# Kernel tuning notes

Hardware: AMD Instinct MI355X
Metric: run time of the kernel (lower is better)

Reference implementation:

```python
import jax, jax.numpy as jnp
import numpy as np
from jax import lax
from jax.scipy.special import logsumexp

LOG2PI = 1.8378770664093453

def _gauss_lp(x, mean, logvar):
    return -0.5 * ((x - mean) ** 2 * jnp.exp(-logvar) + logvar + LOG2PI)

def setup_inputs() -> dict:
    key = jax.random.key(0)
    ks = jax.random.split(key, 12)
    B, T, D, H, X, K, U = 32, 1024, 512, 512, 32, 8, 2
    s = 0.05
    return {
        'ys': jax.random.normal(ks[0], (B, T, D), jnp.float32),
        'us': jax.random.normal(ks[1], (B, T, U), jnp.float32),
        'eps': jax.random.normal(ks[2], (B, T, X), jnp.float32),
        'W1': jax.random.normal(ks[3], (D, H), jnp.float32) * s,
        'b1': jnp.zeros((H,), jnp.float32),
        'Wmu': jax.random.normal(ks[4], (H, X), jnp.float32) * s,
        'bmu': jnp.zeros((X,), jnp.float32),
        'Wlv': jax.random.normal(ks[5], (H, X), jnp.float32) * s,
        'blv': jnp.zeros((X,), jnp.float32),
        'Wz': jax.random.normal(ks[6], (X, K * K), jnp.float32) * s,
        'bz': jnp.zeros((K * K,), jnp.float32),
        'A': jax.random.normal(ks[7], (K, X, X), jnp.float32) * s,
        'Bu': jax.random.normal(ks[8], (K, U, X), jnp.float32) * s,
        'bx': jnp.zeros((K, X), jnp.float32),
        'x_logvar': jnp.zeros((K, X), jnp.float32),
        'x0_mean': jax.random.normal(ks[9], (K, X), jnp.float32) * s,
        'x0_logvar': jnp.zeros((K, X), jnp.float32),
        'C': jax.random.normal(ks[10], (X, D), jnp.float32) * s,
        'd': jnp.zeros((D,), jnp.float32),
        'y_logvar': jnp.zeros((D,), jnp.float32),
        'log_init_z': jnp.zeros((K,), jnp.float32),
    }

def _forward_backward(log_a, log_b, log_init):
    # log_a: [B,T,K,K] with log_a[:,t,j,k] = log p(z_t=j | z_{t-1}=k); log_b: [B,T,K]
    B, T, K = log_b.shape
    la = jnp.moveaxis(log_a[:, 1:], 1, 0)  # [T-1,B,K,K]
    lb = jnp.moveaxis(log_b[:, 1:], 1, 0)  # [T-1,B,K]
    a0 = log_init[None, :] + log_b[:, 0]
    c0 = logsumexp(a0, axis=-1)
    a0 = a0 - c0[:, None]
    def fstep(alpha, ab):
        la_t, lb_t = ab
        a = lb_t + logsumexp(la_t + alpha[:, None, :], axis=-1)
        c = logsumexp(a, axis=-1)
        an = a - c[:, None]
        return an, (an, c)
    _, (alphas, cs) = lax.scan(fstep, a0, (la, lb))
    log_px = c0 + jnp.sum(cs, axis=0)  # [B] log marginal likelihood
    fwd = jnp.concatenate([a0[None], alphas], axis=0)  # [T,B,K]
    betaT = jnp.zeros((B, K), log_b.dtype)
    def bstep(beta, ab):
        la_t, lb_t = ab
        b = logsumexp(la_t + (lb_t + beta)[:, :, None], axis=1)  # sum over next-state j
        b = b - logsumexp(b, axis=-1, keepdims=True)
        return b, b
    _, betas = lax.scan(bstep, betaT, (la, lb), reverse=True)
    bwd = jnp.concatenate([betas, betaT[None]], axis=0)  # [T,B,K]
    lg = fwd + bwd
    log_gamma1 = lg - logsumexp(lg, axis=-1, keepdims=True)
    return jnp.moveaxis(log_gamma1, 0, 1), log_px

def reference(ys, us, eps, W1, b1, Wmu, bmu, Wlv, blv, Wz, bz, A, Bu, bx,
              x_logvar, x0_mean, x0_logvar, C, d, y_logvar, log_init_z):
    B, T, D = ys.shape
    K, X = x0_mean.shape
    # inference net q(x|y): per-step MLP producing Gaussian, reparameterized sample
    h = jnp.tanh(ys @ W1 + b1)
    mu = h @ Wmu + bmu
    lv = h @ Wlv + blv
    x = mu + jnp.exp(0.5 * lv) * eps                        # [B,T,X]
    x_entropy = 0.5 * jnp.sum(eps ** 2 + lv + LOG2PI, -1)   # -log q(x^), [B,T]
    # discrete transition log p(z_t | z_{t-1}, x_{t-1}) with log(eye) prepended at t=0
    logits = (x[:, :-1] @ Wz + bz).reshape(B, T - 1, K, K)
    log_a_t = jax.nn.log_softmax(logits, axis=-2)           # normalize_logprob axis=-2
    log_eye = jnp.log(jnp.eye(K, dtype=ys.dtype) + 1e-10)[None, None]
    log_a = jnp.concatenate([jnp.broadcast_to(log_eye, (B, 1, K, K)), log_a_t], axis=1)
    # continuous likelihood log p(x_t | x_{t-1}, u_t, z_t=k) -> [B,T,K]
    log_b0 = jnp.sum(_gauss_lp(x[:, 0, None, :], x0_mean, x0_logvar), -1)  # [B,K]
    means = (jnp.einsum('btd,kde->btke', x[:, :-1], A)
             + jnp.einsum('btu,kue->btke', us[:, 1:], Bu) + bx)            # [B,T-1,K,X]
    log_bt = jnp.sum(_gauss_lp(x[:, 1:, None, :], means, x_logvar), -1)
    log_b = jnp.concatenate([log_b0[:, None], log_bt], axis=1)
    log_init = jax.nn.log_softmax(log_init_z)
    log_gamma1, log_px = _forward_backward(log_a, log_b, log_init)
    # posterior-weighted generated mean mixed over states, then emission
    xt1_gen = jnp.sum(means * jnp.exp(log_gamma1[:, 1:, :, None]), axis=-2)
    x_gen1 = jnp.concatenate([x[:, :1], xt1_gen], axis=1)
    y_mean = x_gen1 @ C + d
    log_py = jnp.sum(_gauss_lp(ys, y_mean, y_logvar), -1)   # [B,T]
    log_p_xy = log_px + jnp.sum(log_py, -1)                 # [B]
    log_qx = jnp.mean(jnp.sum(x_entropy, 1))
    elbo = jnp.mean(log_p_xy) + log_qx
    return elbo
```

## Files before the change

kernel.cpp:

```cpp
#include <hip/hip_runtime.h>
#include <math.h>

#define LOG2PI 1.8378770664093453f

#define NB 32
#define NT 1024
#define ND 512
#define NH 512
#define NX 32
#define NK 8
#define NU 2

#define NCH 93
#define CHL 11

typedef __attribute__((ext_vector_type(8))) short bf16x8;
typedef __attribute__((ext_vector_type(4))) float f32x4;

__device__ __forceinline__ unsigned short f2bf(float f) {
    unsigned u = __float_as_uint(f);
    unsigned r = (u + 0x7FFF + ((u >> 16) & 1)) >> 16;
    return (unsigned short)r;
}

__device__ __forceinline__ unsigned pack_bf2(float a, float b) {
    unsigned ua = __float_as_uint(a) + 0x8000u;
    unsigned ub = __float_as_uint(b) + 0x8000u;
    return __builtin_amdgcn_perm(ub, ua, 0x07060302);
}

__device__ __forceinline__ float tanh_fast(float v) {
    float t = __expf(2.0f * v);
    return 1.0f - 2.0f * __builtin_amdgcn_rcpf(t + 1.0f);
}

#define DPP_X1 0xB1
#define DPP_X2 0x4E
#define DPP_X3 0x1B
#define DPP_X7 0x141

template <int CTRL>
__device__ __forceinline__ float dppx(float v) {
    return __int_as_float(__builtin_amdgcn_update_dpp(
        0, __float_as_int(v), CTRL, 0xF, 0xF, true));
}

__device__ __forceinline__ float fb_matvec(float4 a0, float4 a1, float v) {
    float p1 = dppx<DPP_X1>(v);
    float p2 = dppx<DPP_X2>(v);
    float p3 = dppx<DPP_X3>(v);
    float p7 = dppx<DPP_X7>(v);
    float p4 = dppx<DPP_X7>(p3);
    float p5 = dppx<DPP_X7>(p2);
    float p6 = dppx<DPP_X7>(p1);
    float c0 = fmaf(a0.y, p1, a0.x * v);
    float c1 = fmaf(a0.w, p3, a0.z * p2);
    float c2 = fmaf(a1.y, p5, a1.x * p4);
    float c3 = fmaf(a1.w, p7, a1.z * p6);
    return (c0 + c1) + (c2 + c3);
}

__device__ __forceinline__ float fb_matvecT(float4 a0, float4 a1, float w) {
    float q0 = a0.x * w;
    float t1 = dppx<DPP_X1>(a0.y * w);
    float t2 = dppx<DPP_X2>(a0.z * w);
    float t3 = dppx<DPP_X3>(a0.w * w);
    float t7 = dppx<DPP_X7>(a1.w * w);
    float t4 = dppx<DPP_X7>(dppx<DPP_X3>(a1.x * w));
    float t5 = dppx<DPP_X7>(dppx<DPP_X2>(a1.y * w));
    float t6 = dppx<DPP_X7>(dppx<DPP_X1>(a1.z * w));
    return ((q0 + t1) + (t2 + t3)) + ((t4 + t5) + (t6 + t7));
}

__device__ __forceinline__ float gsum8(float v) {
    float s = v + dppx<DPP_X1>(v);
    s = s + dppx<DPP_X2>(s);
    s = s + dppx<DPP_X7>(dppx<DPP_X3>(s));
    return s;
}

__device__ __forceinline__ float max8(float4 l0, float4 l1) {
    return fmaxf(fmaxf(fmaxf(l0.x, l0.y), fmaxf(l0.z, l0.w)),
                 fmaxf(fmaxf(l1.x, l1.y), fmaxf(l1.z, l1.w)));
}

__device__ __forceinline__ float lse8_high(float v) {
    float m = v;
    m = fmaxf(m, __shfl_xor(m, 8, 64));
    m = fmaxf(m, __shfl_xor(m, 16, 64));
    m = fmaxf(m, __shfl_xor(m, 32, 64));
    float s = __expf(v - m);
    s += __shfl_xor(s, 8, 64);
    s += __shfl_xor(s, 16, 64);
    s += __shfl_xor(s, 32, 64);
    return m + __logf(s);
}

__global__ __launch_bounds__(256) void k_prep_w(
    const float* __restrict__ W1, const float* __restrict__ Wmu,
    const float* __restrict__ Wlv, const float* __restrict__ C,
    const float* __restrict__ dvec, const float* __restrict__ ylv,
    unsigned short* __restrict__ WT, unsigned short* __restrict__ wmlv,
    unsigned short* __restrict__ W2bf, float* __restrict__ G,
    float* __restrict__ c2x, float* __restrict__ ivbuf)
{
    __shared__ float tile[32][33];
    const int bid = blockIdx.x;
    const int tid = threadIdx.x;
    if (bid < 256) {
        const int bx = (bid & 15) * 32;
        const int by = (bid >> 4) * 32;
        const int tx = tid & 31, ty = tid >> 5;
        for (int i = ty; i < 32; i += 8)
            tile[i][tx] = W1[(size_t)(bx + i) * 512 + by + tx];
        __syncthreads();
        for (int i = ty; i < 32; i += 8)
            WT[(size_t)(by + i) * 512 + bx + tx] = f2bf(tile[tx][i]);
        return;
    }
    if (bid < 288) {
        const int t = bid - 256;
        const float* W = (t >> 4) ? Wlv : Wmu;
        const int base = (t >> 4) * 32;
        const int g = t & 15;
        const int tx = tid & 31, ty = tid >> 5;
        for (int i = ty; i < 32; i += 8)
            tile[i][tx] = W[(size_t)(g * 32 + i) * 32 + tx];
        __syncthreads();
        for (int i = ty; i < 32; i += 8)
            wmlv[(size_t)(base + i) * 512 + g * 32 + tx] = f2bf(tile[tx][i]);
        return;
    }
    if (bid == 320) {
        for (int i = tid; i < 32 * 512; i += 256)
            W2bf[i] = f2bf(C[i] * __expf(-ylv[i & 511]));
        ivbuf[tid] = __expf(-ylv[tid]);
        ivbuf[tid + 256] = __expf(-ylv[tid + 256]);
        return;
    }
    const int x = bid - 288;
    const int y = tid >> 3, seg = tid & 7;
    const float* Cx = &C[(size_t)x * 512];
    const float* Cy = &C[(size_t)y * 512];
    float p = 0.f;
    for (int j = 0; j < 64; ++j) {
        int dcol = seg * 64 + j;
        p = fmaf(Cx[dcol] * __expf(-ylv[dcol]), Cy[dcol], p);
    }
    p = gsum8(p);
    if (seg == 0) G[x * 33 + y] = p;
    if (tid < 8) {
        float q = 0.f;
        for (int j = 0; j < 64; ++j) {
            int dcol = tid * 64 + j;
            q = fmaf(Cx[dcol] * __expf(-ylv[dcol]), dvec[dcol], q);
        }
        q = gsum8(q);
        if (tid == 0) c2x[x] = q;
    }
}

__global__ __launch_bounds__(256) void k_gemm_h_mfma(
    const float* __restrict__ ys,
    const unsigned short* __restrict__ Bbf,
    const float* __restrict__ b1, unsigned short* __restrict__ hb)
{
    __shared__ unsigned short As[128 * 64];
    __shared__ unsigned short Bs[128 * 64];
    const int tid = threadIdx.x;
    const int bm = blockIdx.x * 128;
    const int bn = blockIdx.y * 128;
    const int wid = tid >> 6, lane = tid & 63;
    const int wm = wid >> 1, wn = wid & 1;

    f32x4 acc[4][4];
#pragma unroll
    for (int m = 0; m < 4; ++m)
#pragma unroll
        for (int n = 0; n < 4; ++n)
            acc[m][n] = (f32x4){0.f, 0.f, 0.f, 0.f};

    for (int k0 = 0; k0 < 512; k0 += 64) {
#pragma unroll
        for (int r = 0; r < 4; ++r) {
            int l = tid + r * 256;
            int row = l >> 3, c8 = l & 7;
            int sidx = row * 8 + (c8 ^ (row & 7));
            const float4 f0 = *reinterpret_cast<const float4*>(
                &ys[(size_t)(bm + row) * 512 + k0 + c8 * 8]);
            const float4 f1 = *reinterpret_cast<const float4*>(
                &ys[(size_t)(bm + row) * 512 + k0 + c8 * 8 + 4]);
            uint4 ua;
            ua.x = pack_bf2(f0.x, f0.y);
            ua.y = pack_bf2(f0.z, f0.w);
            ua.z = pack_bf2(f1.x, f1.y);
            ua.w = pack_bf2(f1.z, f1.w);
            *reinterpret_cast<uint4*>(&As[sidx * 8]) = ua;
            uint4 vb = *reinterpret_cast<const uint4*>(
                &Bbf[(size_t)(bn + row) * 512 + k0 + c8 * 8]);
            *reinterpret_cast<uint4*>(&Bs[sidx * 8]) = vb;
        }
        __syncthreads();
#pragma unroll
        for (int kh = 0; kh < 2; ++kh) {
            bf16x8 af[4], bfr[4];
            const int c8r = kh * 4 + (lane >> 4);
#pragma unroll
            for (int m = 0; m < 4; ++m) {
                int rA = wm * 64 + m * 16 + (lane & 15);
                af[m] = *reinterpret_cast<bf16x8*>(
                    &As[rA * 64 + (c8r ^ (rA & 7)) * 8]);
            }
#pragma unroll
            for (int n = 0; n < 4; ++n) {
                int rB = wn * 64 + n * 16 + (lane & 15);
                bfr[n] = *reinterpret_cast<bf16x8*>(
                    &Bs[rB * 64 + (c8r ^ (rB & 7)) * 8]);
            }
#pragma unroll
            for (int m = 0; m < 4; ++m)
#pragma unroll
                for (int n = 0; n < 4; ++n)
                    acc[m][n] = __builtin_amdgcn_mfma_f32_16x16x32_bf16(
                        af[m], bfr[n], acc[m][n], 0, 0, 0);
        }
        __syncthreads();
    }
    float b1v[4];
#pragma unroll
    for (int n = 0; n < 4; ++n)
        b1v[n] = b1[bn + wn * 64 + n * 16 + (lane & 15)];
#pragma unroll
    for (int m = 0; m < 4; ++m) {
#pragma unroll
        for (int q = 0; q < 4; ++q) {
            int row = bm + wm * 64 + m * 16 + (lane >> 4) * 4 + q;
#pragma unroll
            for (int n = 0; n < 4; ++n) {
                int col = bn + wn * 64 + n * 16 + (lane & 15);
                hb[(size_t)row * 512 + col] =
                    f2bf(tanh_fast(acc[m][n][q] + b1v[n]));
            }
        }
    }
}

__global__ __launch_bounds__(256) void k_proj(
    const float* __restrict__ ys, const unsigned short* __restrict__ W2bf,
    const float* __restrict__ dvec, const float* __restrict__ ivbuf,
    float* __restrict__ proj, float* __restrict__ term1)
{
    __shared__ unsigned short As[128 * 64];
    __shared__ unsigned short Bs[32 * 64];
    const int tid = threadIdx.x;
    const int bm = blockIdx.x * 128;
    const int wid = tid >> 6, lane = tid & 63;
    const int c8 = tid & 7;
    f32x4 acc[2][2];
#pragma unroll
    for (int m = 0; m < 2; ++m)
#pragma unroll
        for (int n = 0; n < 2; ++n)
            acc[m][n] = (f32x4){0.f, 0.f, 0.f, 0.f};
    float t1p[4] = {0.f, 0.f, 0.f, 0.f};

    for (int k0 = 0; k0 < 512; k0 += 64) {
        const float4 dv0 = *reinterpret_cast<const float4*>(&dvec[k0 + c8 * 8]);
        const float4 dv1 = *reinterpret_cast<const float4*>(&dvec[k0 + c8 * 8 + 4]);
        const float4 iv0 = *reinterpret_cast<const float4*>(&ivbuf[k0 + c8 * 8]);
        const float4 iv1 = *reinterpret_cast<const float4*>(&ivbuf[k0 + c8 * 8 + 4]);
#pragma unroll
        for (int r = 0; r < 4; ++r) {
            int l = tid + r * 256;
            int row = l >> 3;
            int sidx = row * 8 + (c8 ^ (row & 7));
            const float4 f0 = *reinterpret_cast<const float4*>(
                &ys[(size_t)(bm + row) * 512 + k0 + c8 * 8]);
            const float4 f1 = *reinterpret_cast<const float4*>(
                &ys[(size_t)(bm + row) * 512 + k0 + c8 * 8 + 4]);
            float g0 = f0.x - dv0.x, g1 = f0.y - dv0.y;
            float g2 = f0.z - dv0.z, g3 = f0.w - dv0.w;
            float g4 = f1.x - dv1.x, g5 = f1.y - dv1.y;
            float g6 = f1.z - dv1.z, g7 = f1.w - dv1.w;
            t1p[r] += (g0 * g0 * iv0.x + g1 * g1 * iv0.y)
                    + (g2 * g2 * iv0.z + g3 * g3 * iv0.w)
                    + (g4 * g4 * iv1.x + g5 * g5 * iv1.y)
                    + (g6 * g6 * iv1.z + g7 * g7 * iv1.w);
            uint4 ua;
            ua.x = pack_bf2(f0.x, f0.y);
            ua.y = pack_bf2(f0.z, f0.w);
            ua.z = pack_bf2(f1.x, f1.y);
            ua.w = pack_bf2(f1.z, f1.w);
            *reinterpret_cast<uint4*>(&As[sidx * 8]) = ua;
        }
        {
            int row = tid >> 3;
            int sidx = row * 8 + (c8 ^ (row & 7));
            uint4 v = *reinterpret_cast<const uint4*>(
                &W2bf[(size_t)row * 512 + k0 + c8 * 8]);
            *reinterpret_cast<uint4*>(&Bs[sidx * 8]) = v;
        }
        __syncthreads();
#pragma unroll
        for (int kh = 0; kh < 2; ++kh) {
            const int c8r = kh * 4 + (lane >> 4);
            bf16x8 af[2], bfr[2];
#pragma unroll
            for (int m = 0; m < 2; ++m) {
                int rA = wid * 32 + m * 16 + (lane & 15);
                af[m] = *reinterpret_cast<bf16x8*>(
                    &As[rA * 64 + (c8r ^ (rA & 7)) * 8]);
            }
#pragma unroll
            for (int n = 0; n < 2; ++n) {
                int rB = n * 16 + (lane & 15);
                bfr[n] = *reinterpret_cast<bf16x8*>(
                    &Bs[rB * 64 + (c8r ^ (rB & 7)) * 8]);
            }
#pragma unroll
            for (int m = 0; m < 2; ++m)
#pragma unroll
                for (int n = 0; n < 2; ++n)
                    acc[m][n] = __builtin_amdgcn_mfma_f32_16x16x32_bf16(
                        af[m], bfr[n], acc[m][n], 0, 0, 0);
        }
        __syncthreads();
    }
#pragma unroll
    for (int m = 0; m < 2; ++m)
#pragma unroll
        for (int q = 0; q < 4; ++q) {
            int row = bm + wid * 32 + m * 16 + (lane >> 4) * 4 + q;
#pragma unroll
            for (int n = 0; n < 2; ++n) {
                int col = n * 16 + (lane & 15);
                proj[(size_t)row * 32 + col] = acc[m][n][q];
            }
        }
#pragma unroll
    for (int r = 0; r < 4; ++r) {
        float s = gsum8(t1p[r]);
        if ((tid & 7) == 0) term1[bm + (tid >> 3) + r * 32] = s;
    }
}

__global__ __launch_bounds__(256) void k_mulv_mfma(
    const unsigned short* __restrict__ hbf,
    const unsigned short* __restrict__ Wt,
    const float* __restrict__ bmu, const float* __restrict__ blv,
    const float* __restrict__ eps,
    float* __restrict__ x, float* __restrict__ xent)
{
    __shared__ unsigned short As[128 * 64];
    __shared__ unsigned short Bs[64 * 64];
    const int tid = threadIdx.x;
    const int bm = blockIdx.x * 128;
    const int wid = tid >> 6, lane = tid & 63;
    f32x4 acc[2][4];
#pragma unroll
    for (int m = 0; m < 2; ++m)
#pragma unroll
        for (int n = 0; n < 4; ++n)
            acc[m][n] = (f32x4){0.f, 0.f, 0.f, 0.f};

    for (int k0 = 0; k0 < 512; k0 += 64) {
#pragma unroll
        for (int r = 0; r < 4; ++r) {
            int l = tid + r * 256, row = l >> 3, c8 = l & 7;
            int sidx = row * 8 + (c8 ^ (row & 7));
            uint4 v = *reinterpret_cast<const uint4*>(
                &hbf[(size_t)(bm + row) * 512 + k0 + c8 * 8]);
            *reinterpret_cast<uint4*>(&As[sidx * 8]) = v;
        }
#pragma unroll
        for (int r = 0; r < 2; ++r) {
            int l = tid + r * 256, row = l >> 3, c8 = l & 7;
            int sidx = row * 8 + (c8 ^ (row & 7));
            uint4 v = *reinterpret_cast<const uint4*>(
                &Wt[(size_t)row * 512 + k0 + c8 * 8]);
            *reinterpret_cast<uint4*>(&Bs[sidx * 8]) = v;
        }
        __syncthreads();
#pragma unroll
        for (int kh = 0; kh < 2; ++kh) {
            const int c8r = kh * 4 + (lane >> 4);
            bf16x8 af[2], bfr[4];
#pragma unroll
            for (int m = 0; m < 2; ++m) {
                int rA = wid * 32 + m * 16 + (lane & 15);
                af[m] = *reinterpret_cast<bf16x8*>(
                    &As[rA * 64 + (c8r ^ (rA & 7)) * 8]);
            }
#pragma unroll
            for (int n = 0; n < 4; ++n) {
                int rB = n * 16 + (lane & 15);
                bfr[n] = *reinterpret_cast<bf16x8*>(
                    &Bs[rB * 64 + (c8r ^ (rB & 7)) * 8]);
            }
#pragma unroll
            for (int m = 0; m < 2; ++m)
#pragma unroll
                for (int n = 0; n < 4; ++n)
                    acc[m][n] = __builtin_amdgcn_mfma_f32_16x16x32_bf16(
                        af[m], bfr[n], acc[m][n], 0, 0, 0);
        }
        __syncthreads();
    }
    const int o0 = lane & 15, o1 = 16 + (lane & 15);
    const float bm0 = bmu[o0], bm1 = bmu[o1];
    const float bl0 = blv[o0], bl1 = blv[o1];
#pragma unroll
    for (int m = 0; m < 2; ++m) {
#pragma unroll
        for (int q = 0; q < 4; ++q) {
            int row = bm + wid * 32 + m * 16 + (lane >> 4) * 4 + q;
            float mu0 = acc[m][0][q] + bm0;
            float mu1 = acc[m][1][q] + bm1;
            float lv0 = acc[m][2][q] + bl0;
            float lv1 = acc[m][3][q] + bl1;
            float e0 = eps[(size_t)row * 32 + o0];
            float e1 = eps[(size_t)row * 32 + o1];
            x[(size_t)row * 32 + o0] = mu0 + __expf(0.5f * lv0) * e0;
            x[(size_t)row * 32 + o1] = mu1 + __expf(0.5f * lv1) * e1;
            float pe = (e0 * e0 + lv0) + (e1 * e1 + lv1);
            pe += __shfl_xor(pe, 1, 64);
            pe += __shfl_xor(pe, 2, 64);
            pe += __shfl_xor(pe, 4, 64);
            pe += __shfl_xor(pe, 8, 64);
            if ((lane & 15) == 0)
                xent[row] = 0.5f * (pe + 32.f * LOG2PI);
        }
    }
}

__global__ __launch_bounds__(256) void k_lb(
    const float* __restrict__ x, const float* __restrict__ us,
    const float* __restrict__ Wz, const float* __restrict__ bz,
    const float* __restrict__ A, const float* __restrict__ Bu,
    const float* __restrict__ bx, const float* __restrict__ x_logvar,
    const float* __restrict__ x0_mean, const float* __restrict__ x0_logvar,
    float* __restrict__ ap1, float* __restrict__ log_b)
{
    __shared__ float SM[8192 + 256 + 16];
    const int tid = threadIdx.x;
    const int bid = blockIdx.x;
    if (bid < 1024) {
        float (*xs)[32] = reinterpret_cast<float(*)[32]>(SM);
        const int lane = tid & 63;
        const int wv = tid >> 6;
        const int itemBase = bid * 32;
        {
            int r = tid >> 3, cc = (tid & 7) * 4;
            int item = itemBase + r;
            int src = (item & (NT - 1)) ? item - 1 : item;
            *reinterpret_cast<float4*>(&xs[r][cc]) =
                *reinterpret_cast<const float4*>(&x[(size_t)src * 32 + cc]);
        }
        float wcol[32];
#pragma unroll
        for (int e = 0; e < 32; ++e) wcol[e] = Wz[e * 64 + lane];
        const float bzv = bz[lane];
        __syncthreads();
        const int j = lane >> 3, k = lane & 7;
        for (int i = wv; i < 32; i += 4) {
            int item = itemBase + i;
            if ((item & (NT - 1)) == 0) continue;
            float acc = bzv;
#pragma unroll
            for (int e = 0; e < 32; ++e) acc = fmaf(xs[i][e], wcol[e], acc);
            float lse = lse8_high(acc);
            ap1[(size_t)item * 64 + j * 8 + (j ^ k)] = __expf(acc - lse);
        }
        return;
    }
    if (bid >= 1024 + 4092) {
        const int b = bid - 5116;
        const int k = tid >> 5, xo = tid & 31;
        float xv = x[((size_t)b * NT) * 32 + xo];
        float mm = x0_mean[k * 32 + xo];
        float lvv = x0_logvar[k * 32 + xo];
        float dd = xv - mm;
        float term = -0.5f * (dd * dd * __expf(-lvv) + lvv + LOG2PI);
        for (int m = 16; m; m >>= 1) term += __shfl_down(term, m, 32);
        if (xo == 0) log_b[(size_t)b * NT * 8 + k] = term;
        return;
    }
    float* As = SM;
    float (*xs8)[32] = reinterpret_cast<float(*)[32]>(SM + 8192);
    float (*us8)[2] = reinterpret_cast<float(*)[2]>(SM + 8448);
    const int base = (bid - 1024) * 8;
    for (int i = tid; i < 2048; i += 256)
        reinterpret_cast<float4*>(As)[i] =
            reinterpret_cast<const float4*>(A)[i];
    {
        int row = tid >> 5, xo = tid & 31;
        int item = base + row;
        int b = item / 1023, tm = item - b * 1023;
        xs8[row][xo] = x[((size_t)b * NT + tm) * 32 + xo];
        if (xo < 2) us8[row][xo] = us[((size_t)b * NT + tm + 1) * 2 + xo];
    }
    __syncthreads();
    const int k = tid >> 5, xo = tid & 31;
    const float bxv = bx[k * 32 + xo];
    const float bu0 = Bu[(k * 2 + 0) * 32 + xo];
    const float bu1 = Bu[(k * 2 + 1) * 32 + xo];
    const float lvv = x_logvar[k * 32 + xo];
    const float ivv = __expf(-lvv);
    const float basev = lvv + LOG2PI;
    for (int i = 0; i < 8; ++i) {
        int item = base + i;
        int b = item / 1023, tm = item - b * 1023;
        float acc = fmaf(us8[i][0], bu0, fmaf(us8[i][1], bu1, bxv));
#pragma unroll 8
        for (int e = 0; e < 32; ++e)
            acc = fmaf(xs8[i][e], As[k * 1024 + e * 32 + xo], acc);
        float xv = x[((size_t)b * NT + tm + 1) * 32 + xo];
        float dd = xv - acc;
        float term = dd * dd * ivv + basev;
        for (int m = 16; m; m >>= 1) term += __shfl_down(term, m, 32);
        if (xo == 0)
            log_b[((size_t)b * NT + tm + 1) * 8 + k] = -0.5f * term;
    }
}

__global__ __launch_bounds__(256) void k_fbA(
    const float* __restrict__ ap1, const float* __restrict__ log_b,
    float* __restrict__ Pfx, float* __restrict__ sA)
{
    const int tid = threadIdx.x;
    const int wg = blockIdx.x * 4 + (tid >> 6);
    const int lane = tid & 63;
    const int b = wg / NCH;
    const int c = wg - b * NCH;
    const int j = lane >> 3, k = lane & 7;
    const float* ap = &ap1[(size_t)b * NT * 64];
    const float* lb = &log_b[(size_t)b * NT * 8];
    int t = CHL * c + 1;
    float4 l0 = *reinterpret_cast<const float4*>(&lb[(size_t)t * 8]);
    float4 l1 = *reinterpret_cast<const float4*>(&lb[(size_t)t * 8 + 4]);
    float mm = max8(l0, l1);
    float P = __expf(lb[(size_t)t * 8 + j] - mm) * ap[t * 64 + j * 8 + (j ^ k)];
    float sacc = mm;
    for (int i = 1; i < CHL; ++i) {
        ++t;
        float4 m0 = *reinterpret_cast<const float4*>(&ap[(size_t)t * 64 + j * 8]);
        float4 m1 = *reinterpret_cast<const float4*>(&ap[(size_t)t * 64 + j * 8 + 4]);
        l0 = *reinterpret_cast<const float4*>(&lb[(size_t)t * 8]);
        l1 = *reinterpret_cast<const float4*>(&lb[(size_t)t * 8 + 4]);
        mm = max8(l0, l1);
        float bj = __expf(lb[(size_t)t * 8 + j] - mm);
        sacc += mm;
        float x1 = __shfl_xor(P, 8, 64);
        float x2 = __shfl_xor(P, 16, 64);
        float x3 = __shfl_xor(P, 24, 64);
        float x4 = __shfl_xor(P, 32, 64);
        float x5 = __shfl_xor(P, 40, 64);
        float x6 = __shfl_xor(P, 48, 64);
        float x7 = __shfl_xor(P, 56, 64);
        float c0 = fmaf(m0.y, x1, m0.x * P);
        float c1 = fmaf(m0.w, x3, m0.z * x2);
        float c2 = fmaf(m1.y, x5, m1.x * x4);
        float c3 = fmaf(m1.w, x7, m1.z * x6);
        P = bj * ((c0 + c1) + (c2 + c3));
        if ((i & 3) == 3) {
            float mx = P;
            mx = fmaxf(mx, __shfl_xor(mx, 1, 64));
            mx = fmaxf(mx, __shfl_xor(mx, 2, 64));
            mx = fmaxf(mx, __shfl_xor(mx, 4, 64));
            mx = fmaxf(mx, __shfl_xor(mx, 8, 64));
            mx = fmaxf(mx, __shfl_xor(mx, 16, 64));
            mx = fmaxf(mx, __shfl_xor(mx, 32, 64));
            mx = fmaxf(mx, 1e-30f);
            float r = __builtin_amdgcn_rcpf(mx);
            P *= r;
            sacc -= __logf(r);
        }
    }
    Pfx[((size_t)b * NCH + c) * 64 + j * 8 + (j ^ k)] = P;
    if (lane == 0) sA[b * NCH + c] = sacc;
}

__global__ __launch_bounds__(128) void k_fbB(
    const float* __restrict__ Pfx, const float* __restrict__ sA,
    const float* __restrict__ log_b, const float* __restrict__ log_init_z,
    float* __restrict__ alphaB, float* __restrict__ betaB,
    float* __restrict__ log_px)
{
    const int b = blockIdx.x;
    const int tid = threadIdx.x;
    const int wave = tid >> 6;
    const int lane = tid & 63;
    const int st = lane & 7;
    const float* pf = &Pfx[(size_t)b * NCH * 64];
    if (wave == 0) {
        float liv[8];
        float mz = -1e30f, sz = 0.f;
#pragma unroll
        for (int q = 0; q < 8; ++q) liv[q] = log_init_z[q];
#pragma unroll
        for (int q = 0; q < 8; ++q) mz = fmaxf(mz, liv[q]);
#pragma unroll
        for (int q = 0; q < 8; ++q) sz += __expf(liv[q] - mz);
        const float* lb0 = &log_b[(size_t)b * NT * 8];
        float4 l0 = *reinterpret_cast<const float4*>(lb0);
        float4 l1 = *reinterpret_cast<const float4*>(lb0 + 4);
        float mb0 = max8(l0, l1);
        float alpha = (__expf(liv[st] - mz) / sz) * __expf(lb0[st] - mb0);
        float logS = 0.f, sAsum = 0.f;
        {
            float s = fmaxf(gsum8(alpha), 1e-35f);
            logS += __logf(s);
            alpha *= __builtin_amdgcn_rcpf(s);
        }
        if (lane < 8) alphaB[((size_t)b * (NCH + 1)) * 8 + lane] = alpha;
        for (int c = 0; c < NCH; ++c) {
            float4 a0 = *reinterpret_cast<const float4*>(&pf[(size_t)c * 64 + st * 8]);
            float4 a1 = *reinterpret_cast<const float4*>(&pf[(size_t)c * 64 + st * 8 + 4]);
            alpha = fb_matvec(a0, a1, alpha);
            float s = fmaxf(gsum8(alpha), 1e-35f);
            logS += __logf(s);
            alpha *= __builtin_amdgcn_rcpf(s);
            sAsum += sA[b * NCH + c];
            if (lane < 8) alphaB[((size_t)b * (NCH + 1) + c + 1) * 8 + lane] = alpha;
        }
        if (lane == 0) log_px[b] = mb0 + sAsum + logS;
    } else {
        float beta = 1.f;
        if (lane < 8) betaB[((size_t)b * (NCH + 1) + NCH) * 8 + lane] = 1.f;
        for (int c = NCH - 1; c >= 0; --c) {
            float4 a0 = *reinterpret_cast<const float4*>(&pf[(size_t)c * 64 + st * 8]);
            float4 a1 = *reinterpret_cast<const float4*>(&pf[(size_t)c * 64 + st * 8 + 4]);
            beta = fb_matvecT(a0, a1, beta);
            float s = fmaxf(gsum8(beta), 1e-35f);
            beta *= __builtin_amdgcn_rcpf(s);
            if (lane < 8) betaB[((size_t)b * (NCH + 1) + c) * 8 + lane] = beta;
        }
    }
}

__global__ __launch_bounds__(256) void k_fbC(
    const float* __restrict__ ap1, const float* __restrict__ log_b,
    const float* __restrict__ alphaB, const float* __restrict__ betaB,
    float* __restrict__ gamma)
{
    __shared__ float alphaS[32][CHL][8];
    const int tid = threadIdx.x;
    const int g = tid >> 3;
    const int st = tid & 7;
    const int task = blockIdx.x * 32 + g;
    const int b = task / NCH;
    const int c = task - b * NCH;
    const float* ap = &ap1[(size_t)b * NT * 64];
    const float* lb = &log_b[(size_t)b * NT * 8];
    const int t0 = CHL * c;
    float alpha = alphaB[((size_t)b * (NCH + 1) + c) * 8 + st];
#pragma unroll
    for (int i = 1; i <= CHL; ++i) {
        int t = t0 + i;
        float4 a0 = *reinterpret_cast<const float4*>(&ap[(size_t)t * 64 + st * 8]);
        float4 a1 = *reinterpret_cast<const float4*>(&ap[(size_t)t * 64 + st * 8 + 4]);
        float4 l0 = *reinterpret_cast<const float4*>(&lb[(size_t)t * 8]);
        float4 l1 = *reinterpret_cast<const float4*>(&lb[(size_t)t * 8 + 4]);
        float bv = __expf(lb[(size_t)t * 8 + st] - max8(l0, l1));
        alpha = fb_matvec(a0, a1, alpha) * bv;
        if (i == 5)
            alpha *= __builtin_amdgcn_rcpf(fmaxf(gsum8(alpha), 1e-35f));
        alphaS[g][i - 1][st] = alpha;
    }
    float beta = betaB[((size_t)b * (NCH + 1) + c + 1) * 8 + st];
#pragma unroll
    for (int i = CHL; i >= 1; --i) {
        int t = t0 + i;
        float gv = alphaS[g][i - 1][st] * beta;
        float s = fmaxf(gsum8(gv), 1e-35f);
        gamma[((size_t)b * NT + t) * 8 + st] = gv * __builtin_amdgcn_rcpf(s);
        float4 a0 = *reinterpret_cast<const float4*>(&ap[(size_t)t * 64 + st * 8]);
        float4 a1 = *reinterpret_cast<const float4*>(&ap[(size_t)t * 64 + st * 8 + 4]);
        float4 l0 = *reinterpret_cast<const float4*>(&lb[(size_t)t * 8]);
        float4 l1 = *reinterpret_cast<const float4*>(&lb[(size_t)t * 8 + 4]);
        float bv = __expf(lb[(size_t)t * 8 + st] - max8(l0, l1));
        beta = fb_matvecT(a0, a1, beta * bv);
        if (i == 6)
            beta *= __builtin_amdgcn_rcpf(fmaxf(gsum8(beta), 1e-35f));
    }
    if (c == 0) {
        float a0v = alphaB[((size_t)b * (NCH + 1)) * 8 + st];
        float gv = a0v * beta;
        float s = fmaxf(gsum8(gv), 1e-35f);
        gamma[((size_t)b * NT) * 8 + st] = gv * __builtin_amdgcn_rcpf(s);
    }
}

__global__ __launch_bounds__(256) void k_py(
    const float* __restrict__ x, const float* __restrict__ us,
    const float* __restrict__ A, const float* __restrict__ Bu,
    const float* __restrict__ bx, const float* __restrict__ gamma,
    const float* __restrict__ proj, const float* __restrict__ term1,
    const float* __restrict__ Gm, const float* __restrict__ c2x,
    const float* __restrict__ xent, float* __restrict__ red)
{
    __shared__ float As[8192];
    __shared__ float Gs[32 * 33];
    __shared__ float c2s[32];
    __shared__ float xp8[8][32];
    __shared__ float gs[8][8];
    __shared__ float us8[8][2];
    __shared__ float xgS[8][32];
    const int tid = threadIdx.x;
    const int itemBase = blockIdx.x * 8;
    const int t0 = itemBase & (NT - 1);
    for (int i = tid; i < 2048; i += 256)
        reinterpret_cast<float4*>(As)[i] =
            reinterpret_cast<const float4*>(A)[i];
    for (int i = tid; i < 32 * 33; i += 256) Gs[i] = Gm[i];
    if (tid < 32) c2s[tid] = c2x[tid];
    {
        int it = tid >> 5, xo = tid & 31;
        int t = t0 + it;
        int item = itemBase + it;
        xp8[it][xo] = (t > 0) ? x[((size_t)item - 1) * 32 + xo] : 0.f;
        if (xo < 8) gs[it][xo] = (t > 0) ? gamma[(size_t)item * 8 + xo] : 0.f;
        if (xo < 2) us8[it][xo] = (t > 0) ? us[(size_t)item * 2 + xo] : 0.f;
    }
    __syncthreads();
    const int it = tid >> 5;
    const int xo = tid & 31;
    const int t = t0 + it;
    const int item = itemBase + it;
    float xg;
    if (t == 0) {
        xg = x[(size_t)item * 32 + xo];
    } else {
        xg = 0.f;
#pragma unroll
        for (int k = 0; k < 8; ++k) {
            float acc = bx[k * 32 + xo];
            acc = fmaf(us8[it][0], Bu[(k * 2 + 0) * 32 + xo], acc);
            acc = fmaf(us8[it][1], Bu[(k * 2 + 1) * 32 + xo], acc);
#pragma unroll 8
            for (int e = 0; e < 32; ++e)
                acc = fmaf(xp8[it][e], As[k * 1024 + e * 32 + xo], acc);
            xg = fmaf(gs[it][k], acc, xg);
        }
    }
    xgS[it][xo] = xg;
    __syncthreads();
    float gmv = 0.f;
#pragma unroll 8
    for (int y = 0; y < 32; ++y)
        gmv = fmaf(Gs[xo * 33 + y], xgS[it][y], gmv);
    float val = xg * (proj[(size_t)item * 32 + xo] - c2s[xo] - 0.5f * gmv);
    val += __shfl_xor(val, 1, 64);
    val += __shfl_xor(val, 2, 64);
    val += __shfl_xor(val, 4, 64);
    val += __shfl_xor(val, 8, 64);
    val += __shfl_xor(val, 16, 64);
    if (xo == 0)
        red[item] = -0.5f * term1[item] + val + xent[item];
}

__global__ __launch_bounds__(256) void k_final(
    const float* __restrict__ red, const float* __restrict__ log_px,
    const float* __restrict__ ylv, float* __restrict__ out)
{
    __shared__ float ssum[4];
    __shared__ float ssum2[4];
    const int tid = threadIdx.x;
    float s = 0.f, t = 0.f;
    for (int i = tid; i < NB * NT; i += 256) s += red[i];
    if (tid < NB) s += log_px[tid];
    for (int i = tid; i < 512; i += 256) t += ylv[i] + LOG2PI;
#pragma unroll
    for (int m = 1; m < 64; m <<= 1) {
        s += __shfl_xor(s, m, 64);
        t += __shfl_xor(t, m, 64);
    }
    if ((tid & 63) == 0) { ssum[tid >> 6] = s; ssum2[tid >> 6] = t; }
    __syncthreads();
    if (tid == 0) {
        float S = ssum[0] + ssum[1] + ssum[2] + ssum[3];
        float T = ssum2[0] + ssum2[1] + ssum2[2] + ssum2[3];
        out[0] = S / (float)NB - 512.0f * T;
    }
}

extern "C" void kernel_launch(void* const* d_in, const int* in_sizes, int n_in,
                              void* d_out, int out_size, void* d_ws,
                              size_t ws_size, hipStream_t stream)
{
    const float* ys        = (const float*)d_in[0];
    const float* us        = (const float*)d_in[1];
    const float* eps       = (const float*)d_in[2];
    const float* W1        = (const float*)d_in[3];
    const float* b1        = (const float*)d_in[4];
    const float* Wmu       = (const float*)d_in[5];
    const float* bmu       = (const float*)d_in[6];
    const float* Wlv       = (const float*)d_in[7];
    const float* blv       = (const float*)d_in[8];
    const float* Wz        = (const float*)d_in[9];
    const float* bz        = (const float*)d_in[10];
    const float* A         = (const float*)d_in[11];
    const float* Bu        = (const float*)d_in[12];
    const float* bx        = (const float*)d_in[13];
    const float* x_logvar  = (const float*)d_in[14];
    const float* x0_mean   = (const float*)d_in[15];
    const float* x0_logvar = (const float*)d_in[16];
    const float* C         = (const float*)d_in[17];
    const float* dv        = (const float*)d_in[18];
    const float* y_logvar  = (const float*)d_in[19];
    const float* log_init_z= (const float*)d_in[20];
    float* out = (float*)d_out;

    float* ws = (float*)d_ws;
    float* x      = ws;
    float* xent   = x + 1048576;
    float* ap1    = xent + 32768;
    float* log_b  = ap1 + 2097152;
    float* gam    = log_b + 262144;
    float* log_px = gam + 262144;
    float* red    = log_px + 32;
    float* hbf_f  = red + 32768;
    float* w1t_f  = hbf_f + 8388608;
    float* wmlv_f = w1t_f + 131072;
    float* proj   = wmlv_f + 16384;
    float* term1  = proj + 1048576;
    float* ivbuf  = term1 + 32768;
    float* w2bf_f = ivbuf + 512;
    float* Gm     = w2bf_f + 8192;
    float* c2x    = Gm + 1056;
    float* Pfx    = c2x + 32;
    float* sA     = Pfx + 190464;
    float* alphaB = sA + 2976;
    float* betaB  = alphaB + 24064;

    unsigned short* hbf  = (unsigned short*)hbf_f;
    unsigned short* w1t  = (unsigned short*)w1t_f;
    unsigned short* wmlv = (unsigned short*)wmlv_f;
    unsigned short* w2bf = (unsigned short*)w2bf_f;

    k_prep_w <<<321, 256, 0, stream>>>(W1, Wmu, Wlv, C, dv, y_logvar,
                                       w1t, wmlv, w2bf, Gm, c2x, ivbuf);
    k_gemm_h_mfma<<<dim3(256, 4), 256, 0, stream>>>(ys, w1t, b1, hbf);
    k_proj   <<<256, 256, 0, stream>>>(ys, w2bf, dv, ivbuf, proj, term1);
    k_mulv_mfma<<<256, 256, 0, stream>>>(hbf, wmlv, bmu, blv, eps, x, xent);
    k_lb     <<<5148, 256, 0, stream>>>(x, us, Wz, bz, A, Bu, bx, x_logvar,
                                        x0_mean, x0_logvar, ap1, log_b);
    k_fbA    <<<744, 256, 0, stream>>>(ap1, log_b, Pfx, sA);
    k_fbB    <<<32, 128, 0, stream>>>(Pfx, sA, log_b, log_init_z,
                                      alphaB, betaB, log_px);
    k_fbC    <<<93, 256, 0, stream>>>(ap1, log_b, alphaB, betaB, gam);
    k_py     <<<4096, 256, 0, stream>>>(x, us, A, Bu, bx, gam, proj, term1,
                                        Gm, c2x, xent, red);
    k_final  <<<1, 256, 0, stream>>>(red, log_px, y_logvar, out);
}
```

Measured before the change: 250.5 us.

## Merge proj and mu/logvar GEMMs into one launch; batch items in k_lb and k_py

Combines the k_proj and k_mulv_mfma kernels into one launch, k_pm, that picks its role from the block index. This removes a launch and lets the two independent GEMMs run concurrently. k_lb and k_py now process 32 items per block instead of 8, so the A matrix is staged into shared memory once per 32 items. k_lb also splits the mean computation from a vectorised Gaussian log-prob reduction that goes through shared memory. Several shuffle reductions become DPP-based reductions. The costs are extra barriers and larger shared memory per block, which may lower occupancy.

```diff
diff --git a/kernel.cpp b/kernel.cpp
--- a/kernel.cpp
+++ b/kernel.cpp
@@ -38,6 +38,7 @@
 #define DPP_X2 0x4E
 #define DPP_X3 0x1B
 #define DPP_X7 0x141
+#define DPP_X15 0x140
 
 template <int CTRL>
 __device__ __forceinline__ float dppx(float v) {
@@ -79,6 +80,23 @@
     return s;
 }
 
+__device__ __forceinline__ float gsum16(float v) {
+    float s = v + dppx<DPP_X1>(v);
+    s = s + dppx<DPP_X2>(s);
+    s = s + dppx<DPP_X7>(dppx<DPP_X3>(s));
+    s = s + dppx<DPP_X15>(dppx<DPP_X7>(s));
+    return s;
+}
+
+__device__ __forceinline__ float gsum32(float v) {
+    float s = v + dppx<DPP_X1>(v);
+    s = s + dppx<DPP_X2>(s);
+    s = s + dppx<DPP_X7>(dppx<DPP_X3>(s));
+    s = s + dppx<DPP_X15>(dppx<DPP_X7>(s));
+    s = s + __shfl_xor(s, 16, 64);
+    return s;
+}
+
 __device__ __forceinline__ float max8(float4 l0, float4 l1) {
     return fmaxf(fmaxf(fmaxf(l0.x, l0.y), fmaxf(l0.z, l0.w)),
                  fmaxf(fmaxf(l1.x, l1.y), fmaxf(l1.z, l1.w)));
@@ -86,11 +104,11 @@
 
 __device__ __forceinline__ float lse8_high(float v) {
     float m = v;
-    m = fmaxf(m, __shfl_xor(m, 8, 64));
+    m = fmaxf(m, dppx<DPP_X15>(dppx<DPP_X7>(m)));
     m = fmaxf(m, __shfl_xor(m, 16, 64));
     m = fmaxf(m, __shfl_xor(m, 32, 64));
     float s = __expf(v - m);
-    s += __shfl_xor(s, 8, 64);
+    s += dppx<DPP_X15>(dppx<DPP_X7>(s));
     s += __shfl_xor(s, 16, 64);
     s += __shfl_xor(s, 32, 64);
     return m + __logf(s);
@@ -245,16 +263,99 @@
     }
 }
 
-__global__ __launch_bounds__(256) void k_proj(
+__global__ __launch_bounds__(256) void k_pm(
+    const unsigned short* __restrict__ hbf,
+    const unsigned short* __restrict__ Wt,
+    const float* __restrict__ bmu, const float* __restrict__ blv,
+    const float* __restrict__ eps,
     const float* __restrict__ ys, const unsigned short* __restrict__ W2bf,
     const float* __restrict__ dvec, const float* __restrict__ ivbuf,
+    float* __restrict__ x, float* __restrict__ xent,
     float* __restrict__ proj, float* __restrict__ term1)
 {
-    __shared__ unsigned short As[128 * 64];
-    __shared__ unsigned short Bs[32 * 64];
+    __shared__ unsigned short SMEM[12288];
+    unsigned short* As = SMEM;
+    unsigned short* Bs = SMEM + 8192;
     const int tid = threadIdx.x;
-    const int bm = blockIdx.x * 128;
     const int wid = tid >> 6, lane = tid & 63;
+
+    if (blockIdx.x < 256) {
+        const int bm = blockIdx.x * 128;
+        f32x4 acc[2][4];
+#pragma unroll
+        for (int m = 0; m < 2; ++m)
+#pragma unroll
+            for (int n = 0; n < 4; ++n)
+                acc[m][n] = (f32x4){0.f, 0.f, 0.f, 0.f};
+
+        for (int k0 = 0; k0 < 512; k0 += 64) {
+#pragma unroll
+            for (int r = 0; r < 4; ++r) {
+                int l = tid + r * 256, row = l >> 3, c8 = l & 7;
+                int sidx = row * 8 + (c8 ^ (row & 7));
+                uint4 v = *reinterpret_cast<const uint4*>(
+                    &hbf[(size_t)(bm + row) * 512 + k0 + c8 * 8]);
+                *reinterpret_cast<uint4*>(&As[sidx * 8]) = v;
+            }
+#pragma unroll
+            for (int r = 0; r < 2; ++r) {
+                int l = tid + r * 256, row = l >> 3, c8 = l & 7;
+                int sidx = row * 8 + (c8 ^ (row & 7));
+                uint4 v = *reinterpret_cast<const uint4*>(
+                    &Wt[(size_t)row * 512 + k0 + c8 * 8]);
+                *reinterpret_cast<uint4*>(&Bs[sidx * 8]) = v;
+            }
+            __syncthreads();
+#pragma unroll
+            for (int kh = 0; kh < 2; ++kh) {
+                const int c8r = kh * 4 + (lane >> 4);
+                bf16x8 af[2], bfr[4];
+#pragma unroll
+                for (int m = 0; m < 2; ++m) {
+                    int rA = wid * 32 + m * 16 + (lane & 15);
+                    af[m] = *reinterpret_cast<bf16x8*>(
+                        &As[rA * 64 + (c8r ^ (rA & 7)) * 8]);
+                }
+#pragma unroll
+                for (int n = 0; n < 4; ++n) {
+                    int rB = n * 16 + (lane & 15);
+                    bfr[n] = *reinterpret_cast<bf16x8*>(
+                        &Bs[rB * 64 + (c8r ^ (rB & 7)) * 8]);
+                }
+#pragma unroll
+                for (int m = 0; m < 2; ++m)
+#pragma unroll
+                    for (int n = 0; n < 4; ++n)
+                        acc[m][n] = __builtin_amdgcn_mfma_f32_16x16x32_bf16(
+                            af[m], bfr[n], acc[m][n], 0, 0, 0);
+            }
+            __syncthreads();
+        }
+        const int o0 = lane & 15, o1 = 16 + (lane & 15);
+        const float bm0 = bmu[o0], bm1 = bmu[o1];
+        const float bl0 = blv[o0], bl1 = blv[o1];
+#pragma unroll
+        for (int m = 0; m < 2; ++m) {
+#pragma unroll
+            for (int q = 0; q < 4; ++q) {
+                int row = bm + wid * 32 + m * 16 + (lane >> 4) * 4 + q;
+                float mu0 = acc[m][0][q] + bm0;
+                float mu1 = acc[m][1][q] + bm1;
+                float lv0 = acc[m][2][q] + bl0;
+                float lv1 = acc[m][3][q] + bl1;
+                float e0 = eps[(size_t)row * 32 + o0];
+                float e1 = eps[(size_t)row * 32 + o1];
+                x[(size_t)row * 32 + o0] = mu0 + __expf(0.5f * lv0) * e0;
+                x[(size_t)row * 32 + o1] = mu1 + __expf(0.5f * lv1) * e1;
+                float pe = (e0 * e0 + lv0) + (e1 * e1 + lv1);
+                pe = gsum16(pe);
+                if ((lane & 15) == 0)
+                    xent[row] = 0.5f * (pe + 32.f * LOG2PI);
+            }
+        }
+        return;
+    }
+    const int bm = (blockIdx.x - 256) * 128;
     const int c8 = tid & 7;
     f32x4 acc[2][2];
 #pragma unroll
@@ -344,95 +445,6 @@
     }
 }
 
-__global__ __launch_bounds__(256) void k_mulv_mfma(
-    const unsigned short* __restrict__ hbf,
-    const unsigned short* __restrict__ Wt,
-    const float* __restrict__ bmu, const float* __restrict__ blv,
-    const float* __restrict__ eps,
-    float* __restrict__ x, float* __restrict__ xent)
-{
-    __shared__ unsigned short As[128 * 64];
-    __shared__ unsigned short Bs[64 * 64];
-    const int tid = threadIdx.x;
-    const int bm = blockIdx.x * 128;
-    const int wid = tid >> 6, lane = tid & 63;
-    f32x4 acc[2][4];
-#pragma unroll
-    for (int m = 0; m < 2; ++m)
-#pragma unroll
-        for (int n = 0; n < 4; ++n)
-            acc[m][n] = (f32x4){0.f, 0.f, 0.f, 0.f};
-
-    for (int k0 = 0; k0 < 512; k0 += 64) {
-#pragma unroll
-        for (int r = 0; r < 4; ++r) {
-            int l = tid + r * 256, row = l >> 3, c8 = l & 7;
-            int sidx = row * 8 + (c8 ^ (row & 7));
-            uint4 v = *reinterpret_cast<const uint4*>(
-                &hbf[(size_t)(bm + row) * 512 + k0 + c8 * 8]);
-            *reinterpret_cast<uint4*>(&As[sidx * 8]) = v;
-        }
-#pragma unroll
-        for (int r = 0; r < 2; ++r) {
-            int l = tid + r * 256, row = l >> 3, c8 = l & 7;
-            int sidx = row * 8 + (c8 ^ (row & 7));
-            uint4 v = *reinterpret_cast<const uint4*>(
-                &Wt[(size_t)row * 512 + k0 + c8 * 8]);
-            *reinterpret_cast<uint4*>(&Bs[sidx * 8]) = v;
-        }
-        __syncthreads();
-#pragma unroll
-        for (int kh = 0; kh < 2; ++kh) {
-            const int c8r = kh * 4 + (lane >> 4);
-            bf16x8 af[2], bfr[4];
-#pragma unroll
-            for (int m = 0; m < 2; ++m) {
-                int rA = wid * 32 + m * 16 + (lane & 15);
-                af[m] = *reinterpret_cast<bf16x8*>(
-                    &As[rA * 64 + (c8r ^ (rA & 7)) * 8]);
-            }
-#pragma unroll
-            for (int n = 0; n < 4; ++n) {
-                int rB = n * 16 + (lane & 15);
-                bfr[n] = *reinterpret_cast<bf16x8*>(
-                    &Bs[rB * 64 + (c8r ^ (rB & 7)) * 8]);
-            }
-#pragma unroll
-            for (int m = 0; m < 2; ++m)
-#pragma unroll
-                for (int n = 0; n < 4; ++n)
-                    acc[m][n] = __builtin_amdgcn_mfma_f32_16x16x32_bf16(
-                        af[m], bfr[n], acc[m][n], 0, 0, 0);
-        }
-        __syncthreads();
-    }
-    const int o0 = lane & 15, o1 = 16 + (lane & 15);
-    const float bm0 = bmu[o0], bm1 = bmu[o1];
-    const float bl0 = blv[o0], bl1 = blv[o1];
-#pragma unroll
-    for (int m = 0; m < 2; ++m) {
-#pragma unroll
-        for (int q = 0; q < 4; ++q) {
-            int row = bm + wid * 32 + m * 16 + (lane >> 4) * 4 + q;
-            float mu0 = acc[m][0][q] + bm0;
-            float mu1 = acc[m][1][q] + bm1;
-            float lv0 = acc[m][2][q] + bl0;
-            float lv1 = acc[m][3][q] + bl1;
-            float e0 = eps[(size_t)row * 32 + o0];
-            float e1 = eps[(size_t)row * 32 + o1];
-            x[(size_t)row * 32 + o0] = mu0 + __expf(0.5f * lv0) * e0;
-            x[(size_t)row * 32 + o1] = mu1 + __expf(0.5f * lv1) * e1;
-            float pe = (e0 * e0 + lv0) + (e1 * e1 + lv1);
-            pe += __shfl_xor(pe, 1, 64);
-            pe += __shfl_xor(pe, 2, 64);
-            pe += __shfl_xor(pe, 4, 64);
-            pe += __shfl_xor(pe, 8, 64);
-            if ((lane & 15) == 0)
-                xent[row] = 0.5f * (pe + 32.f * LOG2PI);
-        }
-    }
-}
-
 __global__ __launch_bounds__(256) void k_lb(
     const float* __restrict__ x, const float* __restrict__ us,
     const float* __restrict__ Wz, const float* __restrict__ bz,
@@ -441,7 +453,7 @@
     const float* __restrict__ x0_mean, const float* __restrict__ x0_logvar,
     float* __restrict__ ap1, float* __restrict__ log_b)
 {
-    __shared__ float SM[8192 + 256 + 16];
+    __shared__ float SM[13184];
     const int tid = threadIdx.x;
     const int bid = blockIdx.x;
     if (bid < 1024) {
@@ -473,53 +485,96 @@
         }
         return;
     }
-    if (bid >= 1024 + 4092) {
-        const int b = bid - 5116;
+    if (bid >= 2047) {
+        const int b = bid - 2047;
         const int k = tid >> 5, xo = tid & 31;
         float xv = x[((size_t)b * NT) * 32 + xo];
         float mm = x0_mean[k * 32 + xo];
         float lvv = x0_logvar[k * 32 + xo];
         float dd = xv - mm;
-        float term = -0.5f * (dd * dd * __expf(-lvv) + lvv + LOG2PI);
-        for (int m = 16; m; m >>= 1) term += __shfl_down(term, m, 32);
-        if (xo == 0) log_b[(size_t)b * NT * 8 + k] = term;
+        float term = dd * dd * __expf(-lvv) + lvv + LOG2PI;
+        term = gsum32(term);
+        if (xo == 0) log_b[(size_t)b * NT * 8 + k] = -0.5f * term;
         return;
     }
     float* As = SM;
-    float (*xs8)[32] = reinterpret_cast<float(*)[32]>(SM + 8192);
-    float (*us8)[2] = reinterpret_cast<float(*)[2]>(SM + 8448);
-    const int base = (bid - 1024) * 8;
+    float (*xs)[32] = reinterpret_cast<float(*)[32]>(SM + 8192);
+    float (*xn)[32] = reinterpret_cast<float(*)[32]>(SM + 9216);
+    float (*us2)[2] = reinterpret_cast<float(*)[2]>(SM + 10240);
+    float* ivs = SM + 10304;
+    float* lvp = SM + 10592;
+    float* meanS = SM + 10880;
+    const int base = (bid - 1024) * 32;
     for (int i = tid; i < 2048; i += 256)
         reinterpret_cast<float4*>(As)[i] =
             reinterpret_cast<const float4*>(A)[i];
     {
-        int row = tid >> 5, xo = tid & 31;
-        int item = base + row;
+        int r = tid >> 3, cc = (tid & 7) * 4;
+        int item = base + r;
         int b = item / 1023, tm = item - b * 1023;
-        xs8[row][xo] = x[((size_t)b * NT + tm) * 32 + xo];
-        if (xo < 2) us8[row][xo] = us[((size_t)b * NT + tm + 1) * 2 + xo];
+        *reinterpret_cast<float4*>(&xs[r][cc]) =
+            *reinterpret_cast<const float4*>(&x[((size_t)b * NT + tm) * 32 + cc]);
+        *reinterpret_cast<float4*>(&xn[r][cc]) =
+            *reinterpret_cast<const float4*>(&x[((size_t)b * NT + tm + 1) * 32 + cc]);
+    }
+    if (tid < 64) {
+        int r = tid >> 1, c = tid & 1;
+        int item = base + r;
+        int b = item / 1023, tm = item - b * 1023;
+        us2[r][c] = us[((size_t)b * NT + tm + 1) * 2 + c];
+    }
+    {
+        int k = tid >> 5, xo = tid & 31;
+        float lv = x_logvar[k * 32 + xo];
+        ivs[k * 36 + xo] = __expf(-lv);
+        lvp[k * 36 + xo] = lv + LOG2PI;
     }
     __syncthreads();
     const int k = tid >> 5, xo = tid & 31;
     const float bxv = bx[k * 32 + xo];
     const float bu0 = Bu[(k * 2 + 0) * 32 + xo];
     const float bu1 = Bu[(k * 2 + 1) * 32 + xo];
-    const float lvv = x_logvar[k * 32 + xo];
-    const float ivv = __expf(-lvv);
-    const float basev = lvv + LOG2PI;
-    for (int i = 0; i < 8; ++i) {
-        int item = base + i;
-        int b = item / 1023, tm = item - b * 1023;
-        float acc = fmaf(us8[i][0], bu0, fmaf(us8[i][1], bu1, bxv));
+    const int i2 = tid >> 5;
+    const int k2 = (tid >> 2) & 7, q2 = tid & 3;
+    for (int g = 0; g < 4; ++g) {
+#pragma unroll
+        for (int i = 0; i < 8; ++i) {
+            int r = g * 8 + i;
+            float acc = fmaf(us2[r][0], bu0, fmaf(us2[r][1], bu1, bxv));
 #pragma unroll 8
-        for (int e = 0; e < 32; ++e)
-            acc = fmaf(xs8[i][e], As[k * 1024 + e * 32 + xo], acc);
-        float xv = x[((size_t)b * NT + tm + 1) * 32 + xo];
-        float dd = xv - acc;
-        float term = dd * dd * ivv + basev;
-        for (int m = 16; m; m >>= 1) term += __shfl_down(term, m, 32);
-        if (xo == 0)
-            log_b[((size_t)b * NT + tm + 1) * 8 + k] = -0.5f * term;
+            for (int e = 0; e < 32; ++e)
+                acc = fmaf(xs[r][e], As[k * 1024 + e * 32 + xo], acc);
+            meanS[(i * 8 + k) * 36 + xo] = acc;
+        }
+        __syncthreads();
+        {
+            int r = g * 8 + i2;
+            int item = base + r;
+            int b = item / 1023, tm = item - b * 1023;
+            const float4 xv0 = *reinterpret_cast<const float4*>(&xn[r][q2 * 8]);
+            const float4 xv1 = *reinterpret_cast<const float4*>(&xn[r][q2 * 8 + 4]);
+            const float4 m0 = *reinterpret_cast<const float4*>(
+                &meanS[(i2 * 8 + k2) * 36 + q2 * 8]);
+            const float4 m1 = *reinterpret_cast<const float4*>(
+                &meanS[(i2 * 8 + k2) * 36 + q2 * 8 + 4]);
+            const float4 v0 = *reinterpret_cast<const float4*>(&ivs[k2 * 36 + q2 * 8]);
+            const float4 v1 = *reinterpret_cast<const float4*>(&ivs[k2 * 36 + q2 * 8 + 4]);
+            const float4 p0 = *reinterpret_cast<const float4*>(&lvp[k2 * 36 + q2 * 8]);
+            const float4 p1 = *reinterpret_cast<const float4*>(&lvp[k2 * 36 + q2 * 8 + 4]);
+            float d0 = xv0.x - m0.x, d1 = xv0.y - m0.y;
+            float d2 = xv0.z - m0.z, d3 = xv0.w - m0.w;
+            float d4 = xv1.x - m1.x, d5 = xv1.y - m1.y;
+            float d6 = xv1.z - m1.z, d7 = xv1.w - m1.w;
+            float s = ((d0 * d0 * v0.x + p0.x) + (d1 * d1 * v0.y + p0.y))
+                    + ((d2 * d2 * v0.z + p0.z) + (d3 * d3 * v0.w + p0.w))
+                    + ((d4 * d4 * v1.x + p1.x) + (d5 * d5 * v1.y + p1.y))
+                    + ((d6 * d6 * v1.z + p1.z) + (d7 * d7 * v1.w + p1.w));
+            s += dppx<DPP_X1>(s);
+            s += dppx<DPP_X2>(s);
+            if (q2 == 0)
+                log_b[((size_t)b * NT + tm + 1) * 8 + k2] = -0.5f * s;
+        }
+        __syncthreads();
     }
 }
 
@@ -700,63 +755,71 @@
     const float* __restrict__ xent, float* __restrict__ red)
 {
     __shared__ float As[8192];
-    __shared__ float Gs[32 * 33];
+    __shared__ float Gs[1056];
     __shared__ float c2s[32];
-    __shared__ float xp8[8][32];
-    __shared__ float gs[8][8];
-    __shared__ float us8[8][2];
-    __shared__ float xgS[8][32];
+    __shared__ float xp[32][32];
+    __shared__ float gsm[32][8];
+    __shared__ float us2[32][2];
+    __shared__ float xgS[8 * 36];
     const int tid = threadIdx.x;
-    const int itemBase = blockIdx.x * 8;
+    const int itemBase = blockIdx.x * 32;
     const int t0 = itemBase & (NT - 1);
     for (int i = tid; i < 2048; i += 256)
         reinterpret_cast<float4*>(As)[i] =
             reinterpret_cast<const float4*>(A)[i];
-    for (int i = tid; i < 32 * 33; i += 256) Gs[i] = Gm[i];
+    for (int i = tid; i < 1056; i += 256) Gs[i] = Gm[i];
     if (tid < 32) c2s[tid] = c2x[tid];
     {
-        int it = tid >> 5, xo = tid & 31;
-        int t = t0 + it;
-        int item = itemBase + it;
-        xp8[it][xo] = (t > 0) ? x[((size_t)item - 1) * 32 + xo] : 0.f;
-        if (xo < 8) gs[it][xo] = (t > 0) ? gamma[(size_t)item * 8 + xo] : 0.f;
-        if (xo < 2) us8[it][xo] = (t > 0) ? us[(size_t)item * 2 + xo] : 0.f;
+        int r = tid >> 3, cc = (tid & 7) * 4;
+        int item = itemBase + r;
+        int src = (t0 + r > 0) ? item - 1 : item;
+        *reinterpret_cast<float4*>(&xp[r][cc]) =
+            *reinterpret_cast<const float4*>(&x[(size_t)src * 32 + cc]);
+    }
+    {
+        int r = tid >> 3, kk = tid & 7;
+        int item = itemBase + r;
+        gsm[r][kk] = (t0 + r > 0) ? gamma[(size_t)item * 8 + kk] : 0.f;
+    }
+    if (tid < 64) {
+        int r = tid >> 1, c = tid & 1;
+        int item = itemBase + r;
+        us2[r][c] = (t0 + r > 0) ? us[(size_t)item * 2 + c] : 0.f;
     }
     __syncthreads();
-    const int it = tid >> 5;
-    const int xo = tid & 31;
-    const int t = t0 + it;
-    const int item = itemBase + it;
-    float xg;
-    if (t == 0) {
-        xg = x[(size_t)item * 32 + xo];
-    } else {
-        xg = 0.f;
-#pragma unroll
-        for (int k = 0; k < 8; ++k) {
-            float acc = bx[k * 32 + xo];
-            acc = fmaf(us8[it][0], Bu[(k * 2 + 0) * 32 + xo], acc);
-            acc = fmaf(us8[it][1], Bu[(k * 2 + 1) * 32 + xo], acc);
+    const int it = tid >> 5, xo = tid & 31;
+    for (int g = 0; g < 4; ++g) {
+        const int r = g * 8 + it;
+        const int t = t0 + r;
+        const int item = itemBase + r;
+        float xg;
+        if (t == 0) {
+            xg = x[(size_t)item * 32 + xo];
+        } else {
+            xg = 0.f;
+#pragma unroll
+            for (int kk = 0; kk < 8; ++kk) {
+                float acc = bx[kk * 32 + xo];
+                acc = fmaf(us2[r][0], Bu[(kk * 2 + 0) * 32 + xo], acc);
+                acc = fmaf(us2[r][1], Bu[(kk * 2 + 1) * 32 + xo], acc);
 #pragma unroll 8
-            for (int e = 0; e < 32; ++e)
-                acc = fmaf(xp8[it][e], As[k * 1024 + e * 32 + xo], acc);
-            xg = fmaf(gs[it][k], acc, xg);
-        }
-    }
-    xgS[it][xo] = xg;
-    __syncthreads();
-    float gmv = 0.f;
+                for (int e = 0; e < 32; ++e)
+                    acc = fmaf(xp[r][e], As[kk * 1024 + e * 32 + xo], acc);
+                xg = fmaf(gsm[r][kk], acc, xg);
+            }
+        }
+        xgS[it * 36 + xo] = xg;
+        __syncthreads();
+        float gmv = 0.f;
 #pragma unroll 8
-    for (int y = 0; y < 32; ++y)
-        gmv = fmaf(Gs[xo * 33 + y], xgS[it][y], gmv);
-    float val = xg * (proj[(size_t)item * 32 + xo] - c2s[xo] - 0.5f * gmv);
-    val += __shfl_xor(val, 1, 64);
-    val += __shfl_xor(val, 2, 64);
-    val += __shfl_xor(val, 4, 64);
-    val += __shfl_xor(val, 8, 64);
-    val += __shfl_xor(val, 16, 64);
-    if (xo == 0)
-        red[item] = -0.5f * term1[item] + val + xent[item];
+        for (int y = 0; y < 32; ++y)
+            gmv = fmaf(Gs[xo * 33 + y], xgS[it * 36 + y], gmv);
+        float val = xg * (proj[(size_t)item * 32 + xo] - c2s[xo] - 0.5f * gmv);
+        val = gsum32(val);
+        if (xo == 0)
+            red[item] = -0.5f * term1[item] + val + xent[item];
+        __syncthreads();
+    }
 }
 
 __global__ __launch_bounds__(256) void k_final(
@@ -841,15 +904,16 @@
     k_prep_w <<<321, 256, 0, stream>>>(W1, Wmu, Wlv, C, dv, y_logvar,
                                        w1t, wmlv, w2bf, Gm, c2x, ivbuf);
     k_gemm_h_mfma<<<dim3(256, 4), 256, 0, stream>>>(ys, w1t, b1, hbf);
-    k_proj   <<<256, 256, 0, stream>>>(ys, w2bf, dv, ivbuf, proj, term1);
-    k_mulv_mfma<<<256, 256, 0, stream>>>(hbf, wmlv, bmu, blv, eps, x, xent);
-    k_lb     <<<5148, 256, 0, stream>>>(x, us, Wz, bz, A, Bu, bx, x_logvar,
+    k_pm     <<<512, 256, 0, stream>>>(hbf, wmlv, bmu, blv, eps,
+                                       ys, w2bf, dv, ivbuf,
+                                       x, xent, proj, term1);
+    k_lb     <<<2079, 256, 0, stream>>>(x, us, Wz, bz, A, Bu, bx, x_logvar,
                                         x0_mean, x0_logvar, ap1, log_b);
     k_fbA    <<<744, 256, 0, stream>>>(ap1, log_b, Pfx, sA);
     k_fbB    <<<32, 128, 0, stream>>>(Pfx, sA, log_b, log_init_z,
                                       alphaB, betaB, log_px);
     k_fbC    <<<93, 256, 0, stream>>>(ap1, log_b, alphaB, betaB, gam);
-    k_py     <<<4096, 256, 0, stream>>>(x, us, A, Bu, bx, gam, proj, term1,
+    k_py     <<<1024, 256, 0, stream>>>(x, us, A, Bu, bx, gam, proj, term1,
                                         Gm, c2x, xent, red);
     k_final  <<<1, 256, 0, stream>>>(red, log_px, y_logvar, out);
 }
```

Measured after the change: 233.3 us (median of 2 runs). 6.9% less time.
